# Kernel optimization log

Hardware: AMD Instinct MI355X
Metric: run time of the kernel (lower is better)

## Reference

```python
import jax, jax.numpy as jnp
import numpy as np

N = 50000      # nodes
E = 800000     # edges
IN = 128       # input feature dim
HID = 64       # out_channels per head
HEADS = 2
OUT = 40       # num classes
SLOPE = 0.2    # leaky relu negative slope
EPS = 1e-16    # PyG softmax denominator epsilon


def _xavier(key, shape):
    fan_out, fan_in = shape[0], shape[1]
    a = float(np.sqrt(6.0 / (fan_in + fan_out)))
    return jax.random.uniform(key, shape, minval=-a, maxval=a, dtype=jnp.float32)


def setup_inputs() -> dict:
    key = jax.random.key(0)
    ks = jax.random.split(key, 16)
    x = jax.random.normal(ks[0], (N, IN), dtype=jnp.float32)
    edge_index = jax.random.randint(ks[1], (2, E), 0, N, dtype=jnp.int64)
    # GAT layer 1: lin_l == lin_r (shared), weight [H*C, in], att [C, H]
    W1 = _xavier(ks[2], (HEADS * HID, IN))
    b1 = jnp.zeros((HEADS * HID,), jnp.float32)
    al1 = _xavier(ks[3], (HID, HEADS))
    ar1 = _xavier(ks[4], (HID, HEADS))
    # GAT layer 2: input dim = heads*hidden
    W2 = _xavier(ks[5], (HEADS * HID, HEADS * HID))
    b2 = jnp.zeros((HEADS * HID,), jnp.float32)
    al2 = _xavier(ks[6], (HID, HEADS))
    ar2 = _xavier(ks[7], (HID, HEADS))
    # post_mp: Linear(heads*hid, hid) -> Linear(hid, out)
    Wp1 = _xavier(ks[8], (HID, HEADS * HID))
    bp1 = jnp.zeros((HID,), jnp.float32)
    Wp2 = _xavier(ks[9], (OUT, HID))
    bp2 = jnp.zeros((OUT,), jnp.float32)
    return dict(x=x, edge_index=edge_index, W1=W1, b1=b1, al1=al1, ar1=ar1,
                W2=W2, b2=b2, al2=al2, ar2=ar2, Wp1=Wp1, bp1=bp1, Wp2=Wp2, bp2=bp2)


def gat_layer(x, edge_index, W, b, att_l, att_r):
    """One GAT layer: shared linear, per-edge leaky-relu scores,
    segment-softmax keyed by destination node, scatter-sum."""
    n = x.shape[0]
    xt = (x @ W.T + b).reshape(n, HEADS, HID)          # [N, H, C] (x_l == x_r)
    alpha_l = jnp.einsum('nhc,ch->nh', xt, att_l)      # [N, H]
    alpha_r = jnp.einsum('nhc,ch->nh', xt, att_r)      # [N, H]
    src, dst = edge_index[0], edge_index[1]            # j = source, i = dest
    e = jax.nn.leaky_relu(alpha_r[dst] + alpha_l[src], SLOPE)   # [E, H]
    # segment softmax over edges grouped by destination node
    seg_max = jax.ops.segment_max(e, dst, num_segments=n)       # [N, H]
    ex = jnp.exp(e - seg_max[dst])
    denom = jax.ops.segment_sum(ex, dst, num_segments=n)        # [N, H]
    alpha = ex / (denom[dst] + EPS)                              # [E, H]
    msg = alpha[:, :, None] * xt[src]                            # [E, H, C]
    out = jax.ops.segment_sum(msg, dst, num_segments=n)          # [N, H, C]
    return out.reshape(n, HEADS * HID)


def reference(x, edge_index, W1, b1, al1, ar1, W2, b2, al2, ar2, Wp1, bp1, Wp2, bp2):
    h = jax.nn.relu(gat_layer(x, edge_index, W1, b1, al1, ar1))
    h = jax.nn.relu(gat_layer(h, edge_index, W2, b2, al2, ar2))
    h = h @ Wp1.T + bp1
    h = h @ Wp2.T + bp2
    return jax.nn.log_softmax(h, axis=1)
```

## Files before the change

kernel.cpp:

```cpp
#include <hip/hip_runtime.h>
#include <hip/hip_fp16.h>
#include <cmath>

#define N_NODES 50000
#define N_EDGES 800000
#define F 128
#define OUT_DIM 40
#define SLOPE 0.2f
#define EPS_DEN 1e-16f

#define BK_SHIFT 7
#define BKSZ 128
#define NBK ((N_NODES + BKSZ - 1) / BKSZ)
#define BK_CAP2 2560
#define SC_CHUNK 2500
#define SC_BLOCKS ((N_EDGES + SC_CHUNK - 1) / SC_CHUNK)

typedef _Float16 half8 __attribute__((ext_vector_type(8)));
typedef float floatx4 __attribute__((ext_vector_type(4)));

__device__ inline float4 load4(const float* p) { return *(const float4*)p; }
__device__ inline float4 load4(const __half* p) {
  uint2 u = *(const uint2*)p;
  float2 a = __half22float2(*(__half2*)&u.x);
  float2 b = __half22float2(*(__half2*)&u.y);
  return make_float4(a.x, a.y, b.x, b.y);
}

template <typename T>
__global__ __launch_bounds__(256) void gemm_mfma(const T* __restrict__ A,
    const float* __restrict__ W, const float* __restrict__ b,
    const float* __restrict__ attl, const float* __restrict__ attr,
    __half* __restrict__ Ch, float* __restrict__ al, float* __restrict__ ar,
    int nrows) {
  __shared__ __half Ah[128][40];
  __shared__ __half Bh[128][40];
  int tid = threadIdx.x;
  int lane = tid & 63, wid = tid >> 6;
  int quad = lane >> 4, col = lane & 15;
  int r0 = blockIdx.x * 128;
  int rowhalf = wid >> 1, colhalf = wid & 1;
  floatx4 acc[4][4] = {};
  for (int kc = 0; kc < 128; kc += 32) {
    for (int i = tid; i < 512; i += 256) {
      int row = i >> 2, seg = i & 3;
      int gr = r0 + row;
      float4 v0, v1;
      if (gr < nrows) {
        const T* p = A + (size_t)gr * 128 + kc + seg * 8;
        v0 = load4(p); v1 = load4(p + 4);
      } else { v0 = make_float4(0.f,0.f,0.f,0.f); v1 = v0; }
      __half2 h0 = __floats2half2_rn(v0.x, v0.y), h1 = __floats2half2_rn(v0.z, v0.w);
      __half2 h2 = __floats2half2_rn(v1.x, v1.y), h3 = __floats2half2_rn(v1.z, v1.w);
      uint4 pk; pk.x = *(unsigned*)&h0; pk.y = *(unsigned*)&h1;
      pk.z = *(unsigned*)&h2; pk.w = *(unsigned*)&h3;
      *(uint4*)&Ah[row][seg * 8] = pk;
      const float* q = W + (size_t)row * 128 + kc + seg * 8;
      float4 w0 = *(const float4*)q, w1 = *(const float4*)(q + 4);
      __half2 g0 = __floats2half2_rn(w0.x, w0.y), g1 = __floats2half2_rn(w0.z, w0.w);
      __half2 g2 = __floats2half2_rn(w1.x, w1.y), g3 = __floats2half2_rn(w1.z, w1.w);
      uint4 qk; qk.x = *(unsigned*)&g0; qk.y = *(unsigned*)&g1;
      qk.z = *(unsigned*)&g2; qk.w = *(unsigned*)&g3;
      *(uint4*)&Bh[row][seg * 8] = qk;
    }
    __syncthreads();
    half8 afr[4], bfr[4];
#pragma unroll
    for (int rt = 0; rt < 4; ++rt)
      afr[rt] = *(const half8*)&Ah[rowhalf * 64 + rt * 16 + col][quad * 8];
#pragma unroll
    for (int ct = 0; ct < 4; ++ct)
      bfr[ct] = *(const half8*)&Bh[colhalf * 64 + ct * 16 + col][quad * 8];
#pragma unroll
    for (int rt = 0; rt < 4; ++rt)
#pragma unroll
      for (int ct = 0; ct < 4; ++ct)
        acc[rt][ct] = __builtin_amdgcn_mfma_f32_16x16x32_f16(afr[rt], bfr[ct],
                                                             acc[rt][ct], 0, 0, 0);
    __syncthreads();
  }
  int head = colhalf;
  float bj[4], wl4[4], wr4[4];
#pragma unroll
  for (int ct = 0; ct < 4; ++ct) {
    int c = ct * 16 + col;
    bj[ct] = b[head * 64 + c];
    wl4[ct] = attl[c * 2 + head];
    wr4[ct] = attr[c * 2 + head];
  }
#pragma unroll
  for (int rt = 0; rt < 4; ++rt) {
#pragma unroll
    for (int reg = 0; reg < 4; ++reg) {
      int gr = r0 + rowhalf * 64 + rt * 16 + quad * 4 + reg;
      bool ok = gr < nrows;
      float pl = 0.f, pr = 0.f;
#pragma unroll
      for (int ct = 0; ct < 4; ++ct) {
        float v = acc[rt][ct][reg] + bj[ct];
        pl += v * wl4[ct]; pr += v * wr4[ct];
        if (ok) Ch[(size_t)gr * F + head * 64 + ct * 16 + col] = __float2half(v);
      }
      pl += __shfl_xor(pl, 1, 64); pr += __shfl_xor(pr, 1, 64);
      pl += __shfl_xor(pl, 2, 64); pr += __shfl_xor(pr, 2, 64);
      pl += __shfl_xor(pl, 4, 64); pr += __shfl_xor(pr, 4, 64);
      pl += __shfl_xor(pl, 8, 64); pr += __shfl_xor(pr, 8, 64);
      if (ok && col == 0) { al[gr * 2 + head] = pl; ar[gr * 2 + head] = pr; }
    }
  }
}

__global__ __launch_bounds__(256) void bucket_scatter(const int* __restrict__ ei,
    int* __restrict__ bcur, int* __restrict__ pairs) {
  __shared__ int   sd[SC_CHUNK];
  __shared__ short sb[SC_CHUNK];
  __shared__ int h[NBK], lofs[NBK];
  int tid = threadIdx.x;
  for (int i = tid; i < NBK; i += 256) h[i] = 0;
  __syncthreads();
  int base = blockIdx.x * SC_CHUNK;
  int end = base + SC_CHUNK; if (end > N_EDGES) end = N_EDGES;
  int cnt = end - base;
  for (int e = base + tid; e < end; e += 256) {
    int s = ei[e];
    int d = ei[N_EDGES + e];
    int b = d >> BK_SHIFT;
    sd[e - base] = (s << BK_SHIFT) | (d & (BKSZ - 1));
    sb[e - base] = (short)b;
    atomicAdd(&h[b], 1);
  }
  __syncthreads();
  for (int i = tid; i < NBK; i += 256)
    if (h[i]) { lofs[i] = i * BK_CAP2 + atomicAdd(&bcur[i], h[i]); h[i] = 0; }
  __syncthreads();
  for (int i = tid; i < cnt; i += 256) {
    int b = sb[i];
    int pos = lofs[b] + atomicAdd(&h[b], 1);
    pairs[pos] = sd[i];
  }
}

__global__ __launch_bounds__(256) void local_sort(const int* __restrict__ bcur,
    const int* __restrict__ pairs, int* __restrict__ rowstart,
    int* __restrict__ rowend, int* __restrict__ srcs) {
  __shared__ int buf[BK_CAP2];
  __shared__ int sorted[BK_CAP2];
  __shared__ int hist[BKSZ];
  __shared__ int cur[BKSZ];
  int tid = threadIdx.x;
  int b = blockIdx.x;
  int base = b * BK_CAP2;
  int cnt = bcur[b];
  if (cnt > BK_CAP2) cnt = BK_CAP2;
  if (tid < BKSZ) hist[tid] = 0;
  __syncthreads();
  for (int i = tid; i < cnt; i += 256) {
    int p = pairs[base + i];
    buf[i] = p;
    atomicAdd(&hist[p & (BKSZ - 1)], 1);
  }
  __syncthreads();
  if (tid < 64) {
    int lane = tid;
    int carry = 0;
#pragma unroll
    for (int c = 0; c < BKSZ; c += 64) {
      int v = hist[c + lane];
      int x = v;
#pragma unroll
      for (int off = 1; off < 64; off <<= 1) {
        int t = __shfl_up(x, off, 64);
        if (lane >= off) x += t;
      }
      int excl = carry + x - v;
      cur[c + lane] = excl;
      int node = b * BKSZ + c + lane;
      if (node < N_NODES) {
        rowstart[node] = base + excl;
        rowend[node]   = base + excl + v;
      }
      carry += __shfl(x, 63, 64);
    }
  }
  __syncthreads();
  for (int i = tid; i < cnt; i += 256) {
    int p = buf[i];
    int pos = atomicAdd(&cur[p & (BKSZ - 1)], 1);
    sorted[pos] = p >> BK_SHIFT;
  }
  __syncthreads();
  for (int i = tid; i < cnt; i += 256)
    srcs[base + i] = sorted[i];
}

__global__ __launch_bounds__(256) void aggregate_kernel(const int* __restrict__ rowstart,
    const int* __restrict__ rowend, const int* __restrict__ srcs,
    const float* __restrict__ al, const float* __restrict__ ar,
    const __half* __restrict__ xh, __half* __restrict__ out, int n) {
  __shared__ float ebuf[4][2][64];
  __shared__ int   sbuf[4][64];
  int tid = threadIdx.x;
  int wid = tid >> 6, lane = tid & 63;
  int g = lane >> 4, q = lane & 15;
  int head = q >> 3;
  int node = blockIdx.x * 4 + wid;
  if (node >= n) return;
  int start = rowstart[node], end = rowend[node];
  float2 arv = *(const float2*)(ar + (size_t)node * 2);
  float ar0 = arv.x, ar1 = arv.y;
  const float* wrow = &ebuf[wid][head][0];
  const __half* xbase = xh + q * 8;
  float acc[8] = {};
  float dl0 = 0.f, dl1 = 0.f;
  for (int c = start; c < end; c += 64) {
    int j = c + lane;
    float e0 = 0.f, e1 = 0.f; int soff = 0;
    if (j < end) {
      int s = srcs[j];
      soff = s << BK_SHIFT;
      float2 a = *(const float2*)(al + (size_t)s * 2);
      float s0 = a.x + ar0; s0 = (s0 > 0.f) ? s0 : SLOPE * s0;
      float s1 = a.y + ar1; s1 = (s1 > 0.f) ? s1 : SLOPE * s1;
      e0 = __expf(s0); e1 = __expf(s1);
    }
    dl0 += e0; dl1 += e1;
    ebuf[wid][0][lane] = e0; ebuf[wid][1][lane] = e1; sbuf[wid][lane] = soff;
    __builtin_amdgcn_wave_barrier();
    int cend = end - c; if (cend > 64) cend = 64;
#pragma unroll 4
    for (int t = 0; t < cend; t += 4) {
      int te = t + g;
      if (te < cend) {
        int so = sbuf[wid][te];
        float w = wrow[te];
        uint4 u = *(const uint4*)(xbase + so);
        const __half2* hh = (const __half2*)&u;
        float2 f0 = __half22float2(hh[0]);
        float2 f1 = __half22float2(hh[1]);
        float2 f2 = __half22float2(hh[2]);
        float2 f3 = __half22float2(hh[3]);
        acc[0] += w * f0.x; acc[1] += w * f0.y;
        acc[2] += w * f1.x; acc[3] += w * f1.y;
        acc[4] += w * f2.x; acc[5] += w * f2.y;
        acc[6] += w * f3.x; acc[7] += w * f3.y;
      }
    }
    __builtin_amdgcn_wave_barrier();
  }
#pragma unroll
  for (int off = 32; off > 0; off >>= 1) {
    dl0 += __shfl_xor(dl0, off, 64);
    dl1 += __shfl_xor(dl1, off, 64);
  }
#pragma unroll
  for (int k = 0; k < 8; ++k) {
    acc[k] += __shfl_xor(acc[k], 16, 64);
    acc[k] += __shfl_xor(acc[k], 32, 64);
  }
  if (g == 0) {
    float d = (head == 0) ? dl0 : dl1;
    float inv = 1.f / (d + EPS_DEN);
    __half2 o0 = __floats2half2_rn(fmaxf(acc[0] * inv, 0.f), fmaxf(acc[1] * inv, 0.f));
    __half2 o1 = __floats2half2_rn(fmaxf(acc[2] * inv, 0.f), fmaxf(acc[3] * inv, 0.f));
    __half2 o2 = __floats2half2_rn(fmaxf(acc[4] * inv, 0.f), fmaxf(acc[5] * inv, 0.f));
    __half2 o3 = __floats2half2_rn(fmaxf(acc[6] * inv, 0.f), fmaxf(acc[7] * inv, 0.f));
    uint4 pack;
    pack.x = *(unsigned*)&o0; pack.y = *(unsigned*)&o1;
    pack.z = *(unsigned*)&o2; pack.w = *(unsigned*)&o3;
    *(uint4*)(out + (size_t)node * F + q * 8) = pack;
  }
}

__global__ void combine_kernel(const float* __restrict__ Wp1, const float* __restrict__ bp1,
    const float* __restrict__ Wp2, const float* __restrict__ bp2,
    __half* __restrict__ Wch, float* __restrict__ bc) {
  int idx = blockIdx.x * 256 + threadIdx.x;
  if (blockIdx.x < 24) {
    int o = idx >> 7, k = idx & 127;
    float s = 0.f;
    if (o < OUT_DIM) {
#pragma unroll 8
      for (int j = 0; j < 64; ++j) s += Wp2[o * 64 + j] * Wp1[j * 128 + k];
    }
    Wch[o * 128 + k] = __float2half(s);
  } else if (threadIdx.x < 48) {
    int o = threadIdx.x;
    if (o < OUT_DIM) {
      float s = bp2[o];
      for (int j = 0; j < 64; ++j) s += Wp2[o * 64 + j] * bp1[j];
      bc[o] = s;
    } else {
      bc[o] = -1e30f;
    }
  }
}

__global__ __launch_bounds__(256) void post_mfma(const __half* __restrict__ hb,
    const __half* __restrict__ Wch, const float* __restrict__ bc,
    float* __restrict__ out, int n) {
  int tid = threadIdx.x;
  int lane = tid & 63, wid = tid >> 6;
  int quad = lane >> 4, col = lane & 15;
  int base = blockIdx.x * 64 + wid * 16;
  int arow = base + col;
  int asafe = (arow < n) ? arow : (n - 1);
  floatx4 acc[3] = {};
#pragma unroll
  for (int kc = 0; kc < 128; kc += 32) {
    half8 afr = *(const half8*)(hb + (size_t)asafe * F + kc + quad * 8);
#pragma unroll
    for (int ct = 0; ct < 3; ++ct) {
      half8 bfr = *(const half8*)(Wch + (size_t)(ct * 16 + col) * 128 + kc + quad * 8);
      acc[ct] = __builtin_amdgcn_mfma_f32_16x16x32_f16(afr, bfr, acc[ct], 0, 0, 0);
    }
  }
  float bcv[3];
#pragma unroll
  for (int ct = 0; ct < 3; ++ct) bcv[ct] = bc[ct * 16 + col];
#pragma unroll
  for (int reg = 0; reg < 4; ++reg) {
    int row = base + quad * 4 + reg;
    float z[3], m = -INFINITY;
#pragma unroll
    for (int ct = 0; ct < 3; ++ct) { z[ct] = acc[ct][reg] + bcv[ct]; m = fmaxf(m, z[ct]); }
    m = fmaxf(m, __shfl_xor(m, 1, 64));
    m = fmaxf(m, __shfl_xor(m, 2, 64));
    m = fmaxf(m, __shfl_xor(m, 4, 64));
    m = fmaxf(m, __shfl_xor(m, 8, 64));
    float s = 0.f;
#pragma unroll
    for (int ct = 0; ct < 3; ++ct) s += __expf(z[ct] - m);
    s += __shfl_xor(s, 1, 64);
    s += __shfl_xor(s, 2, 64);
    s += __shfl_xor(s, 4, 64);
    s += __shfl_xor(s, 8, 64);
    float ls = logf(s);
    if (row < n) {
#pragma unroll
      for (int ct = 0; ct < 3; ++ct) {
        int o = ct * 16 + col;
        if (o < OUT_DIM) out[(size_t)row * OUT_DIM + o] = z[ct] - m - ls;
      }
    }
  }
}

extern "C" void kernel_launch(void* const* d_in, const int* in_sizes, int n_in,
                              void* d_out, int out_size, void* d_ws, size_t ws_size,
                              hipStream_t stream) {
  const float* x   = (const float*)d_in[0];
  const int*   ei  = (const int*)d_in[1];
  const float* W1  = (const float*)d_in[2];
  const float* b1  = (const float*)d_in[3];
  const float* al1 = (const float*)d_in[4];
  const float* ar1 = (const float*)d_in[5];
  const float* W2  = (const float*)d_in[6];
  const float* b2  = (const float*)d_in[7];
  const float* al2 = (const float*)d_in[8];
  const float* ar2 = (const float*)d_in[9];
  const float* Wp1 = (const float*)d_in[10];
  const float* bp1 = (const float*)d_in[11];
  const float* Wp2 = (const float*)d_in[12];
  const float* bp2 = (const float*)d_in[13];
  float* out = (float*)d_out;

  float* al    = (float*)d_ws;
  float* ar    = al + (size_t)N_NODES * 2;
  __half* Wch  = (__half*)(ar + (size_t)N_NODES * 2);
  float* bc    = (float*)(Wch + 48 * 128);
  int* rowstart= (int*)(bc + 48);
  int* rowend  = rowstart + N_NODES;
  int* bcur    = rowend + N_NODES;
  int* srcs    = bcur + NBK + 1;
  int* pairs   = srcs + NBK * BK_CAP2;
  uintptr_t pp = ((uintptr_t)(pairs + NBK * BK_CAP2) + 255) & ~(uintptr_t)255;
  __half* xh   = (__half*)pp;
  __half* hb   = xh + (size_t)N_NODES * F;

  hipMemsetAsync(bcur, 0, NBK * sizeof(int), stream);
  bucket_scatter<<<SC_BLOCKS, 256, 0, stream>>>(ei, bcur, pairs);
  local_sort<<<NBK, 256, 0, stream>>>(bcur, pairs, rowstart, rowend, srcs);
  combine_kernel<<<25, 256, 0, stream>>>(Wp1, bp1, Wp2, bp2, Wch, bc);

  int ggrid = (N_NODES + 127) / 128;
  int nwgrid = (N_NODES + 3) / 4;

  gemm_mfma<float><<<ggrid, 256, 0, stream>>>(x, W1, b1, al1, ar1, xh, al, ar, N_NODES);
  aggregate_kernel<<<nwgrid, 256, 0, stream>>>(rowstart, rowend, srcs, al, ar, xh, hb, N_NODES);
  gemm_mfma<__half><<<ggrid, 256, 0, stream>>>(hb, W2, b2, al2, ar2, xh, al, ar, N_NODES);
  aggregate_kernel<<<nwgrid, 256, 0, stream>>>(rowstart, rowend, srcs, al, ar, xh, hb, N_NODES);
  post_mfma<<<(N_NODES + 63) / 64, 256, 0, stream>>>(hb, Wch, bc, out, N_NODES);
}
```

Baseline: 237.2 us.

## Fuse all GAT stages into one persistent megakernel with grid barriers

Merges edge bucketing, the post-MLP weight combine, layer-1 GEMM, sorting, both aggregations, the layer-2 GEMM and the post MLP into one persistent kernel. The phases are separated by a software grid barrier built on atomics. Edge scatter, the weight combine and the first GEMM now share one phase, so independent work runs together. This removes per-launch overhead and idle gaps between the separate launches. The cost is that the spin barrier only works if every block is resident; the grid size comes from an occupancy query and is capped at 1024 blocks.

```diff
diff --git a/kernel.cpp b/kernel.cpp
--- a/kernel.cpp
+++ b/kernel.cpp
@@ -15,9 +15,39 @@
 #define BK_CAP2 2560
 #define SC_CHUNK 2500
 #define SC_BLOCKS ((N_EDGES + SC_CHUNK - 1) / SC_CHUNK)
+#define GEMM_TILES ((N_NODES + 127) / 128)
+#define AGG_ITEMS ((N_NODES + 3) / 4)
+#define POST_TILES ((N_NODES + 63) / 64)
+#define P0_ITEMS (SC_BLOCKS + 25 + GEMM_TILES)
+#define SMEM_BYTES 21504
 
 typedef _Float16 half8 __attribute__((ext_vector_type(8)));
 typedef float floatx4 __attribute__((ext_vector_type(4)));
+
+struct ScatterS { int sd[SC_CHUNK]; short sb[SC_CHUNK]; int h[NBK]; int lofs[NBK]; };
+struct SortS    { int buf[BK_CAP2]; int sorted[BK_CAP2]; int hist[BKSZ]; int cur[BKSZ]; };
+struct GemmS    { __half Ah[128][40]; __half Bh[128][40]; };
+struct AggS     { float ebuf[4][2][64]; int sbuf[4][64]; };
+static_assert(sizeof(ScatterS) <= SMEM_BYTES, "scatter LDS");
+static_assert(sizeof(SortS)    <= SMEM_BYTES, "sort LDS");
+static_assert(sizeof(GemmS)    <= SMEM_BYTES, "gemm LDS");
+static_assert(sizeof(AggS)     <= SMEM_BYTES, "agg LDS");
+
+__device__ __forceinline__ void grid_barrier(int* cnt, int* gen) {
+  __syncthreads();
+  if (threadIdx.x == 0) {
+    __threadfence();
+    int g = atomicAdd(gen, 0);
+    if (atomicAdd(cnt, 1) == (int)gridDim.x - 1) {
+      atomicExch(cnt, 0);
+      atomicAdd(gen, 1);
+    } else {
+      while (atomicAdd(gen, 0) == g) __builtin_amdgcn_s_sleep(2);
+    }
+    __threadfence();
+  }
+  __syncthreads();
+}
 
 __device__ inline float4 load4(const float* p) { return *(const float4*)p; }
 __device__ inline float4 load4(const __half* p) {
@@ -27,18 +57,118 @@
   return make_float4(a.x, a.y, b.x, b.y);
 }
 
+__device__ __forceinline__ void scatter_phase(const int* __restrict__ ei,
+    int* __restrict__ bcur, int* __restrict__ pairs, int it, int tid, char* smem_) {
+  ScatterS* S = (ScatterS*)smem_;
+  for (int i = tid; i < NBK; i += 256) S->h[i] = 0;
+  __syncthreads();
+  int base = it * SC_CHUNK;
+  int end = base + SC_CHUNK; if (end > N_EDGES) end = N_EDGES;
+  int cnt = end - base;
+  for (int e = base + tid; e < end; e += 256) {
+    int s = ei[e];
+    int d = ei[N_EDGES + e];
+    int b = d >> BK_SHIFT;
+    S->sd[e - base] = (s << BK_SHIFT) | (d & (BKSZ - 1));
+    S->sb[e - base] = (short)b;
+    atomicAdd(&S->h[b], 1);
+  }
+  __syncthreads();
+  for (int i = tid; i < NBK; i += 256)
+    if (S->h[i]) { S->lofs[i] = i * BK_CAP2 + atomicAdd(&bcur[i], S->h[i]); S->h[i] = 0; }
+  __syncthreads();
+  for (int i = tid; i < cnt; i += 256) {
+    int b = S->sb[i];
+    int pos = S->lofs[b] + atomicAdd(&S->h[b], 1);
+    pairs[pos] = S->sd[i];
+  }
+  __syncthreads();
+}
+
+__device__ __forceinline__ void combine_phase(const float* __restrict__ Wp1,
+    const float* __restrict__ bp1, const float* __restrict__ Wp2,
+    const float* __restrict__ bp2, __half* __restrict__ Wch,
+    float* __restrict__ bc, int it, int tid) {
+  if (it < 24) {
+    int idx = it * 256 + tid;
+    int o = idx >> 7, k = idx & 127;
+    float s = 0.f;
+    if (o < OUT_DIM) {
+#pragma unroll 8
+      for (int j = 0; j < 64; ++j) s += Wp2[o * 64 + j] * Wp1[j * 128 + k];
+    }
+    Wch[o * 128 + k] = __float2half(s);
+  } else if (tid < 48) {
+    int o = tid;
+    if (o < OUT_DIM) {
+      float s = bp2[o];
+      for (int j = 0; j < 64; ++j) s += Wp2[o * 64 + j] * bp1[j];
+      bc[o] = s;
+    } else {
+      bc[o] = -1e30f;
+    }
+  }
+}
+
+__device__ __forceinline__ void sort_phase(const int* __restrict__ bcur,
+    const int* __restrict__ pairs, int* __restrict__ rowstart,
+    int* __restrict__ rowend, int* __restrict__ srcs, int b, int tid, char* smem_) {
+  SortS* S = (SortS*)smem_;
+  int base = b * BK_CAP2;
+  int cnt = bcur[b];
+  if (cnt > BK_CAP2) cnt = BK_CAP2;
+  if (tid < BKSZ) S->hist[tid] = 0;
+  __syncthreads();
+  for (int i = tid; i < cnt; i += 256) {
+    int p = pairs[base + i];
+    S->buf[i] = p;
+    atomicAdd(&S->hist[p & (BKSZ - 1)], 1);
+  }
+  __syncthreads();
+  if (tid < 64) {
+    int lane = tid;
+    int carry = 0;
+#pragma unroll
+    for (int c = 0; c < BKSZ; c += 64) {
+      int v = S->hist[c + lane];
+      int x = v;
+#pragma unroll
+      for (int off = 1; off < 64; off <<= 1) {
+        int t = __shfl_up(x, off, 64);
+        if (lane >= off) x += t;
+      }
+      int excl = carry + x - v;
+      S->cur[c + lane] = excl;
+      int node = b * BKSZ + c + lane;
+      if (node < N_NODES) {
+        rowstart[node] = base + excl;
+        rowend[node]   = base + excl + v;
+      }
+      carry += __shfl(x, 63, 64);
+    }
+  }
+  __syncthreads();
+  for (int i = tid; i < cnt; i += 256) {
+    int p = S->buf[i];
+    int pos = atomicAdd(&S->cur[p & (BKSZ - 1)], 1);
+    S->sorted[pos] = p >> BK_SHIFT;
+  }
+  __syncthreads();
+  for (int i = tid; i < cnt; i += 256)
+    srcs[base + i] = S->sorted[i];
+  __syncthreads();
+}
+
 template <typename T>
-__global__ __launch_bounds__(256) void gemm_mfma(const T* __restrict__ A,
+__device__ __forceinline__ void gemm_phase(const T* __restrict__ A,
     const float* __restrict__ W, const float* __restrict__ b,
     const float* __restrict__ attl, const float* __restrict__ attr,
     __half* __restrict__ Ch, float* __restrict__ al, float* __restrict__ ar,
-    int nrows) {
-  __shared__ __half Ah[128][40];
-  __shared__ __half Bh[128][40];
-  int tid = threadIdx.x;
+    int nrows, int tile, int tid, char* smem_) {
+  GemmS* S = (GemmS*)smem_;
   int lane = tid & 63, wid = tid >> 6;
   int quad = lane >> 4, col = lane & 15;
-  int r0 = blockIdx.x * 128;
+  int r0 = tile * 128;
   int rowhalf = wid >> 1, colhalf = wid & 1;
   floatx4 acc[4][4] = {};
   for (int kc = 0; kc < 128; kc += 32) {
@@ -54,23 +184,23 @@
       __half2 h2 = __floats2half2_rn(v1.x, v1.y), h3 = __floats2half2_rn(v1.z, v1.w);
       uint4 pk; pk.x = *(unsigned*)&h0; pk.y = *(unsigned*)&h1;
       pk.z = *(unsigned*)&h2; pk.w = *(unsigned*)&h3;
-      *(uint4*)&Ah[row][seg * 8] = pk;
+      *(uint4*)&S->Ah[row][seg * 8] = pk;
       const float* q = W + (size_t)row * 128 + kc + seg * 8;
       float4 w0 = *(const float4*)q, w1 = *(const float4*)(q + 4);
       __half2 g0 = __floats2half2_rn(w0.x, w0.y), g1 = __floats2half2_rn(w0.z, w0.w);
       __half2 g2 = __floats2half2_rn(w1.x, w1.y), g3 = __floats2half2_rn(w1.z, w1.w);
       uint4 qk; qk.x = *(unsigned*)&g0; qk.y = *(unsigned*)&g1;
       qk.z = *(unsigned*)&g2; qk.w = *(unsigned*)&g3;
-      *(uint4*)&Bh[row][seg * 8] = qk;
+      *(uint4*)&S->Bh[row][seg * 8] = qk;
     }
     __syncthreads();
     half8 afr[4], bfr[4];
 #pragma unroll
     for (int rt = 0; rt < 4; ++rt)
-      afr[rt] = *(const half8*)&Ah[rowhalf * 64 + rt * 16 + col][quad * 8];
+      afr[rt] = *(const half8*)&S->Ah[rowhalf * 64 + rt * 16 + col][quad * 8];
 #pragma unroll
     for (int ct = 0; ct < 4; ++ct)
-      bfr[ct] = *(const half8*)&Bh[colhalf * 64 + ct * 16 + col][quad * 8];
+      bfr[ct] = *(const half8*)&S->Bh[colhalf * 64 + ct * 16 + col][quad * 8];
 #pragma unroll
     for (int rt = 0; rt < 4; ++rt)
 #pragma unroll
@@ -110,105 +240,21 @@
   }
 }
 
-__global__ __launch_bounds__(256) void bucket_scatter(const int* __restrict__ ei,
-    int* __restrict__ bcur, int* __restrict__ pairs) {
-  __shared__ int   sd[SC_CHUNK];
-  __shared__ short sb[SC_CHUNK];
-  __shared__ int h[NBK], lofs[NBK];
-  int tid = threadIdx.x;
-  for (int i = tid; i < NBK; i += 256) h[i] = 0;
-  __syncthreads();
-  int base = blockIdx.x * SC_CHUNK;
-  int end = base + SC_CHUNK; if (end > N_EDGES) end = N_EDGES;
-  int cnt = end - base;
-  for (int e = base + tid; e < end; e += 256) {
-    int s = ei[e];
-    int d = ei[N_EDGES + e];
-    int b = d >> BK_SHIFT;
-    sd[e - base] = (s << BK_SHIFT) | (d & (BKSZ - 1));
-    sb[e - base] = (short)b;
-    atomicAdd(&h[b], 1);
-  }
-  __syncthreads();
-  for (int i = tid; i < NBK; i += 256)
-    if (h[i]) { lofs[i] = i * BK_CAP2 + atomicAdd(&bcur[i], h[i]); h[i] = 0; }
-  __syncthreads();
-  for (int i = tid; i < cnt; i += 256) {
-    int b = sb[i];
-    int pos = lofs[b] + atomicAdd(&h[b], 1);
-    pairs[pos] = sd[i];
-  }
-}
-
-__global__ __launch_bounds__(256) void local_sort(const int* __restrict__ bcur,
-    const int* __restrict__ pairs, int* __restrict__ rowstart,
-    int* __restrict__ rowend, int* __restrict__ srcs) {
-  __shared__ int buf[BK_CAP2];
-  __shared__ int sorted[BK_CAP2];
-  __shared__ int hist[BKSZ];
-  __shared__ int cur[BKSZ];
-  int tid = threadIdx.x;
-  int b = blockIdx.x;
-  int base = b * BK_CAP2;
-  int cnt = bcur[b];
-  if (cnt > BK_CAP2) cnt = BK_CAP2;
-  if (tid < BKSZ) hist[tid] = 0;
-  __syncthreads();
-  for (int i = tid; i < cnt; i += 256) {
-    int p = pairs[base + i];
-    buf[i] = p;
-    atomicAdd(&hist[p & (BKSZ - 1)], 1);
-  }
-  __syncthreads();
-  if (tid < 64) {
-    int lane = tid;
-    int carry = 0;
-#pragma unroll
-    for (int c = 0; c < BKSZ; c += 64) {
-      int v = hist[c + lane];
-      int x = v;
-#pragma unroll
-      for (int off = 1; off < 64; off <<= 1) {
-        int t = __shfl_up(x, off, 64);
-        if (lane >= off) x += t;
-      }
-      int excl = carry + x - v;
-      cur[c + lane] = excl;
-      int node = b * BKSZ + c + lane;
-      if (node < N_NODES) {
-        rowstart[node] = base + excl;
-        rowend[node]   = base + excl + v;
-      }
-      carry += __shfl(x, 63, 64);
-    }
-  }
-  __syncthreads();
-  for (int i = tid; i < cnt; i += 256) {
-    int p = buf[i];
-    int pos = atomicAdd(&cur[p & (BKSZ - 1)], 1);
-    sorted[pos] = p >> BK_SHIFT;
-  }
-  __syncthreads();
-  for (int i = tid; i < cnt; i += 256)
-    srcs[base + i] = sorted[i];
-}
-
-__global__ __launch_bounds__(256) void aggregate_kernel(const int* __restrict__ rowstart,
+__device__ __forceinline__ void agg_phase(const int* __restrict__ rowstart,
     const int* __restrict__ rowend, const int* __restrict__ srcs,
     const float* __restrict__ al, const float* __restrict__ ar,
-    const __half* __restrict__ xh, __half* __restrict__ out, int n) {
-  __shared__ float ebuf[4][2][64];
-  __shared__ int   sbuf[4][64];
-  int tid = threadIdx.x;
+    const __half* __restrict__ xh, __half* __restrict__ out,
+    int item, int tid, char* smem_) {
+  AggS* S = (AggS*)smem_;
   int wid = tid >> 6, lane = tid & 63;
   int g = lane >> 4, q = lane & 15;
   int head = q >> 3;
-  int node = blockIdx.x * 4 + wid;
-  if (node >= n) return;
+  int node = item * 4 + wid;
+  if (node >= N_NODES) return;
   int start = rowstart[node], end = rowend[node];
   float2 arv = *(const float2*)(ar + (size_t)node * 2);
   float ar0 = arv.x, ar1 = arv.y;
-  const float* wrow = &ebuf[wid][head][0];
+  const float* wrow = &S->ebuf[wid][head][0];
   const __half* xbase = xh + q * 8;
   float acc[8] = {};
   float dl0 = 0.f, dl1 = 0.f;
@@ -224,14 +270,14 @@
       e0 = __expf(s0); e1 = __expf(s1);
     }
     dl0 += e0; dl1 += e1;
-    ebuf[wid][0][lane] = e0; ebuf[wid][1][lane] = e1; sbuf[wid][lane] = soff;
+    S->ebuf[wid][0][lane] = e0; S->ebuf[wid][1][lane] = e1; S->sbuf[wid][lane] = soff;
     __builtin_amdgcn_wave_barrier();
     int cend = end - c; if (cend > 64) cend = 64;
 #pragma unroll 4
     for (int t = 0; t < cend; t += 4) {
       int te = t + g;
       if (te < cend) {
-        int so = sbuf[wid][te];
+        int so = S->sbuf[wid][te];
         float w = wrow[te];
         uint4 u = *(const uint4*)(xbase + so);
         const __half2* hh = (const __half2*)&u;
@@ -271,39 +317,14 @@
   }
 }
 
-__global__ void combine_kernel(const float* __restrict__ Wp1, const float* __restrict__ bp1,
-    const float* __restrict__ Wp2, const float* __restrict__ bp2,
-    __half* __restrict__ Wch, float* __restrict__ bc) {
-  int idx = blockIdx.x * 256 + threadIdx.x;
-  if (blockIdx.x < 24) {
-    int o = idx >> 7, k = idx & 127;
-    float s = 0.f;
-    if (o < OUT_DIM) {
-#pragma unroll 8
-      for (int j = 0; j < 64; ++j) s += Wp2[o * 64 + j] * Wp1[j * 128 + k];
-    }
-    Wch[o * 128 + k] = __float2half(s);
-  } else if (threadIdx.x < 48) {
-    int o = threadIdx.x;
-    if (o < OUT_DIM) {
-      float s = bp2[o];
-      for (int j = 0; j < 64; ++j) s += Wp2[o * 64 + j] * bp1[j];
-      bc[o] = s;
-    } else {
-      bc[o] = -1e30f;
-    }
-  }
-}
-
-__global__ __launch_bounds__(256) void post_mfma(const __half* __restrict__ hb,
+__device__ __forceinline__ void post_phase(const __half* __restrict__ hb,
     const __half* __restrict__ Wch, const float* __restrict__ bc,
-    float* __restrict__ out, int n) {
-  int tid = threadIdx.x;
+    float* __restrict__ out, int it, int tid) {
   int lane = tid & 63, wid = tid >> 6;
   int quad = lane >> 4, col = lane & 15;
-  int base = blockIdx.x * 64 + wid * 16;
+  int base = it * 64 + wid * 16;
   int arow = base + col;
-  int asafe = (arow < n) ? arow : (n - 1);
+  int asafe = (arow < N_NODES) ? arow : (N_NODES - 1);
   floatx4 acc[3] = {};
 #pragma unroll
   for (int kc = 0; kc < 128; kc += 32) {
@@ -335,7 +356,7 @@
     s += __shfl_xor(s, 4, 64);
     s += __shfl_xor(s, 8, 64);
     float ls = logf(s);
-    if (row < n) {
+    if (row < N_NODES) {
 #pragma unroll
       for (int ct = 0; ct < 3; ++ct) {
         int o = ct * 16 + col;
@@ -343,6 +364,58 @@
       }
     }
   }
+}
+
+__global__ __launch_bounds__(256, 4) void mega(
+    const float* __restrict__ x, const int* __restrict__ ei,
+    const float* __restrict__ W1, const float* __restrict__ b1,
+    const float* __restrict__ al1, const float* __restrict__ ar1,
+    const float* __restrict__ W2, const float* __restrict__ b2,
+    const float* __restrict__ al2, const float* __restrict__ ar2,
+    const float* __restrict__ Wp1, const float* __restrict__ bp1,
+    const float* __restrict__ Wp2, const float* __restrict__ bp2,
+    float* __restrict__ out,
+    float* __restrict__ al, float* __restrict__ ar,
+    __half* __restrict__ Wch, float* __restrict__ bc,
+    int* __restrict__ rowstart, int* __restrict__ rowend,
+    int* __restrict__ bar, int* __restrict__ bcur,
+    int* __restrict__ srcs, int* __restrict__ pairs,
+    __half* __restrict__ xh, __half* __restrict__ hb) {
+  __shared__ __align__(16) char smem[SMEM_BYTES];
+  int tid = threadIdx.x;
+  int bid = blockIdx.x;
+  int nb  = gridDim.x;
+  int* cnt = bar;
+  int* gen = bar + 1;
+
+  for (int it = bid; it < P0_ITEMS; it += nb) {
+    if (it < SC_BLOCKS) scatter_phase(ei, bcur, pairs, it, tid, smem);
+    else if (it < SC_BLOCKS + 25)
+      combine_phase(Wp1, bp1, Wp2, bp2, Wch, bc, it - SC_BLOCKS, tid);
+    else
+      gemm_phase<float>(x, W1, b1, al1, ar1, xh, al, ar, N_NODES,
+                        it - SC_BLOCKS - 25, tid, smem);
+  }
+  grid_barrier(cnt, gen);
+
+  for (int it = bid; it < NBK; it += nb)
+    sort_phase(bcur, pairs, rowstart, rowend, srcs, it, tid, smem);
+  grid_barrier(cnt, gen);
+
+  for (int it = bid; it < AGG_ITEMS; it += nb)
+    agg_phase(rowstart, rowend, srcs, al, ar, xh, hb, it, tid, smem);
+  grid_barrier(cnt, gen);
+
+  for (int it = bid; it < GEMM_TILES; it += nb)
+    gemm_phase<__half>(hb, W2, b2, al2, ar2, xh, al, ar, N_NODES, it, tid, smem);
+  grid_barrier(cnt, gen);
+
+  for (int it = bid; it < AGG_ITEMS; it += nb)
+    agg_phase(rowstart, rowend, srcs, al, ar, xh, hb, it, tid, smem);
+  grid_barrier(cnt, gen);
+
+  for (int it = bid; it < POST_TILES; it += nb)
+    post_phase(hb, Wch, bc, out, it, tid);
 }
 
 extern "C" void kernel_launch(void* const* d_in, const int* in_sizes, int n_in,
@@ -370,24 +443,23 @@
   float* bc    = (float*)(Wch + 48 * 128);
   int* rowstart= (int*)(bc + 48);
   int* rowend  = rowstart + N_NODES;
-  int* bcur    = rowend + N_NODES;
-  int* srcs    = bcur + NBK + 1;
+  int* bar     = rowend + N_NODES;
+  int* bcur    = bar + 8;
+  int* srcs    = bcur + NBK;
   int* pairs   = srcs + NBK * BK_CAP2;
   uintptr_t pp = ((uintptr_t)(pairs + NBK * BK_CAP2) + 255) & ~(uintptr_t)255;
   __half* xh   = (__half*)pp;
   __half* hb   = xh + (size_t)N_NODES * F;
 
-  hipMemsetAsync(bcur, 0, NBK * sizeof(int), stream);
-  bucket_scatter<<<SC_BLOCKS, 256, 0, stream>>>(ei, bcur, pairs);
-  local_sort<<<NBK, 256, 0, stream>>>(bcur, pairs, rowstart, rowend, srcs);
-  combine_kernel<<<25, 256, 0, stream>>>(Wp1, bp1, Wp2, bp2, Wch, bc);
-
-  int ggrid = (N_NODES + 127) / 128;
-  int nwgrid = (N_NODES + 3) / 4;
-
-  gemm_mfma<float><<<ggrid, 256, 0, stream>>>(x, W1, b1, al1, ar1, xh, al, ar, N_NODES);
-  aggregate_kernel<<<nwgrid, 256, 0, stream>>>(rowstart, rowend, srcs, al, ar, xh, hb, N_NODES);
-  gemm_mfma<__half><<<ggrid, 256, 0, stream>>>(hb, W2, b2, al2, ar2, xh, al, ar, N_NODES);
-  aggregate_kernel<<<nwgrid, 256, 0, stream>>>(rowstart, rowend, srcs, al, ar, xh, hb, N_NODES);
-  post_mfma<<<(N_NODES + 63) / 64, 256, 0, stream>>>(hb, Wch, bc, out, N_NODES);
-}
+  int maxB = 0;
+  if (hipOccupancyMaxActiveBlocksPerMultiprocessor(&maxB, (const void*)mega,
+                                                   256, 0) != hipSuccess || maxB < 1)
+    maxB = 2;
+  int nb = maxB * 256;
+  if (nb > 1024) nb = 1024;
+
+  hipMemsetAsync(bar, 0, (8 + NBK) * sizeof(int), stream);
+  mega<<<nb, 256, 0, stream>>>(x, ei, W1, b1, al1, ar1, W2, b2, al2, ar2,
+                               Wp1, bp1, Wp2, bp2, out, al, ar, Wch, bc,
+                               rowstart, rowend, bar, bcur, srcs, pairs, xh, hb);
+}
```

Measured after the change: 617.9 us. 2.61x slower.

## Merge edge scatter, weight combine and first GEMM into one launch

Applied to the files above, without the earlier changes.

The bucket scatter, post-MLP weight combine and layer-1 GEMM are independent, so they now run as one kernel whose block index picks which phase to execute, with shared memory reused through a union-sized byte buffer. This removes two kernel launches and lets the GEMM tiles run alongside the atomic-heavy scatter instead of after it. In exchange every block reserves the larger shared-memory footprint, which may lower occupancy for the GEMM blocks.

```diff
diff --git a/kernel.cpp b/kernel.cpp
--- a/kernel.cpp
+++ b/kernel.cpp
@@ -15,9 +15,17 @@
 #define BK_CAP2 2560
 #define SC_CHUNK 2500
 #define SC_BLOCKS ((N_EDGES + SC_CHUNK - 1) / SC_CHUNK)
+#define GEMM_TILES ((N_NODES + 127) / 128)
+#define A_BLOCKS (SC_BLOCKS + 25 + GEMM_TILES)
+#define SMEM_BYTES 21504
 
 typedef _Float16 half8 __attribute__((ext_vector_type(8)));
 typedef float floatx4 __attribute__((ext_vector_type(4)));
+
+struct ScatterS { int sd[SC_CHUNK]; short sb[SC_CHUNK]; int h[NBK]; int lofs[NBK]; };
+struct GemmS    { __half Ah[128][40]; __half Bh[128][40]; };
+static_assert(sizeof(ScatterS) <= SMEM_BYTES, "scatter LDS");
+static_assert(sizeof(GemmS)    <= SMEM_BYTES, "gemm LDS");
 
 __device__ inline float4 load4(const float* p) { return *(const float4*)p; }
 __device__ inline float4 load4(const __half* p) {
@@ -27,18 +35,68 @@
   return make_float4(a.x, a.y, b.x, b.y);
 }
 
+__device__ __forceinline__ void scatter_phase(const int* __restrict__ ei,
+    int* __restrict__ bcur, int* __restrict__ pairs, int it, int tid, char* smem_) {
+  ScatterS* S = (ScatterS*)smem_;
+  for (int i = tid; i < NBK; i += 256) S->h[i] = 0;
+  __syncthreads();
+  int base = it * SC_CHUNK;
+  int end = base + SC_CHUNK; if (end > N_EDGES) end = N_EDGES;
+  int cnt = end - base;
+  for (int e = base + tid; e < end; e += 256) {
+    int s = ei[e];
+    int d = ei[N_EDGES + e];
+    int b = d >> BK_SHIFT;
+    S->sd[e - base] = (s << BK_SHIFT) | (d & (BKSZ - 1));
+    S->sb[e - base] = (short)b;
+    atomicAdd(&S->h[b], 1);
+  }
+  __syncthreads();
+  for (int i = tid; i < NBK; i += 256)
+    if (S->h[i]) { S->lofs[i] = i * BK_CAP2 + atomicAdd(&bcur[i], S->h[i]); S->h[i] = 0; }
+  __syncthreads();
+  for (int i = tid; i < cnt; i += 256) {
+    int b = S->sb[i];
+    int pos = S->lofs[b] + atomicAdd(&S->h[b], 1);
+    pairs[pos] = S->sd[i];
+  }
+}
+
+__device__ __forceinline__ void combine_phase(const float* __restrict__ Wp1,
+    const float* __restrict__ bp1, const float* __restrict__ Wp2,
+    const float* __restrict__ bp2, __half* __restrict__ Wch,
+    float* __restrict__ bc, int it, int tid) {
+  if (it < 24) {
+    int idx = it * 256 + tid;
+    int o = idx >> 7, k = idx & 127;
+    float s = 0.f;
+    if (o < OUT_DIM) {
+#pragma unroll 8
+      for (int j = 0; j < 64; ++j) s += Wp2[o * 64 + j] * Wp1[j * 128 + k];
+    }
+    Wch[o * 128 + k] = __float2half(s);
+  } else if (tid < 48) {
+    int o = tid;
+    if (o < OUT_DIM) {
+      float s = bp2[o];
+      for (int j = 0; j < 64; ++j) s += Wp2[o * 64 + j] * bp1[j];
+      bc[o] = s;
+    } else {
+      bc[o] = -1e30f;
+    }
+  }
+}
+
 template <typename T>
-__global__ __launch_bounds__(256) void gemm_mfma(const T* __restrict__ A,
+__device__ __forceinline__ void gemm_phase(const T* __restrict__ A,
     const float* __restrict__ W, const float* __restrict__ b,
     const float* __restrict__ attl, const float* __restrict__ attr,
     __half* __restrict__ Ch, float* __restrict__ al, float* __restrict__ ar,
-    int nrows) {
-  __shared__ __half Ah[128][40];
-  __shared__ __half Bh[128][40];
-  int tid = threadIdx.x;
+    int nrows, int tile, int tid, char* smem_) {
+  GemmS* S = (GemmS*)smem_;
   int lane = tid & 63, wid = tid >> 6;
   int quad = lane >> 4, col = lane & 15;
-  int r0 = blockIdx.x * 128;
+  int r0 = tile * 128;
   int rowhalf = wid >> 1, colhalf = wid & 1;
   floatx4 acc[4][4] = {};
   for (int kc = 0; kc < 128; kc += 32) {
@@ -54,23 +112,23 @@
       __half2 h2 = __floats2half2_rn(v1.x, v1.y), h3 = __floats2half2_rn(v1.z, v1.w);
       uint4 pk; pk.x = *(unsigned*)&h0; pk.y = *(unsigned*)&h1;
       pk.z = *(unsigned*)&h2; pk.w = *(unsigned*)&h3;
-      *(uint4*)&Ah[row][seg * 8] = pk;
+      *(uint4*)&S->Ah[row][seg * 8] = pk;
       const float* q = W + (size_t)row * 128 + kc + seg * 8;
       float4 w0 = *(const float4*)q, w1 = *(const float4*)(q + 4);
       __half2 g0 = __floats2half2_rn(w0.x, w0.y), g1 = __floats2half2_rn(w0.z, w0.w);
       __half2 g2 = __floats2half2_rn(w1.x, w1.y), g3 = __floats2half2_rn(w1.z, w1.w);
       uint4 qk; qk.x = *(unsigned*)&g0; qk.y = *(unsigned*)&g1;
       qk.z = *(unsigned*)&g2; qk.w = *(unsigned*)&g3;
-      *(uint4*)&Bh[row][seg * 8] = qk;
+      *(uint4*)&S->Bh[row][seg * 8] = qk;
     }
     __syncthreads();
     half8 afr[4], bfr[4];
 #pragma unroll
     for (int rt = 0; rt < 4; ++rt)
-      afr[rt] = *(const half8*)&Ah[rowhalf * 64 + rt * 16 + col][quad * 8];
+      afr[rt] = *(const half8*)&S->Ah[rowhalf * 64 + rt * 16 + col][quad * 8];
 #pragma unroll
     for (int ct = 0; ct < 4; ++ct)
-      bfr[ct] = *(const half8*)&Bh[colhalf * 64 + ct * 16 + col][quad * 8];
+      bfr[ct] = *(const half8*)&S->Bh[colhalf * 64 + ct * 16 + col][quad * 8];
 #pragma unroll
     for (int rt = 0; rt < 4; ++rt)
 #pragma unroll
@@ -110,34 +168,34 @@
   }
 }
 
-__global__ __launch_bounds__(256) void bucket_scatter(const int* __restrict__ ei,
-    int* __restrict__ bcur, int* __restrict__ pairs) {
-  __shared__ int   sd[SC_CHUNK];
-  __shared__ short sb[SC_CHUNK];
-  __shared__ int h[NBK], lofs[NBK];
-  int tid = threadIdx.x;
-  for (int i = tid; i < NBK; i += 256) h[i] = 0;
-  __syncthreads();
-  int base = blockIdx.x * SC_CHUNK;
-  int end = base + SC_CHUNK; if (end > N_EDGES) end = N_EDGES;
-  int cnt = end - base;
-  for (int e = base + tid; e < end; e += 256) {
-    int s = ei[e];
-    int d = ei[N_EDGES + e];
-    int b = d >> BK_SHIFT;
-    sd[e - base] = (s << BK_SHIFT) | (d & (BKSZ - 1));
-    sb[e - base] = (short)b;
-    atomicAdd(&h[b], 1);
-  }
-  __syncthreads();
-  for (int i = tid; i < NBK; i += 256)
-    if (h[i]) { lofs[i] = i * BK_CAP2 + atomicAdd(&bcur[i], h[i]); h[i] = 0; }
-  __syncthreads();
-  for (int i = tid; i < cnt; i += 256) {
-    int b = sb[i];
-    int pos = lofs[b] + atomicAdd(&h[b], 1);
-    pairs[pos] = sd[i];
-  }
+__global__ __launch_bounds__(256) void kernelA(const int* __restrict__ ei,
+    int* __restrict__ bcur, int* __restrict__ pairs,
+    const float* __restrict__ Wp1, const float* __restrict__ bp1,
+    const float* __restrict__ Wp2, const float* __restrict__ bp2,
+    __half* __restrict__ Wch, float* __restrict__ bc,
+    const float* __restrict__ x, const float* __restrict__ W1,
+    const float* __restrict__ b1, const float* __restrict__ al1,
+    const float* __restrict__ ar1, __half* __restrict__ xh,
+    float* __restrict__ al, float* __restrict__ ar) {
+  __shared__ __align__(16) char smem[SMEM_BYTES];
+  int bid = blockIdx.x, tid = threadIdx.x;
+  if (bid < SC_BLOCKS) {
+    scatter_phase(ei, bcur, pairs, bid, tid, smem);
+  } else if (bid < SC_BLOCKS + 25) {
+    combine_phase(Wp1, bp1, Wp2, bp2, Wch, bc, bid - SC_BLOCKS, tid);
+  } else {
+    gemm_phase<float>(x, W1, b1, al1, ar1, xh, al, ar, N_NODES,
+                      bid - SC_BLOCKS - 25, tid, smem);
+  }
+}
+
+__global__ __launch_bounds__(256) void gemm2_kernel(const __half* __restrict__ hb,
+    const float* __restrict__ W2, const float* __restrict__ b2,
+    const float* __restrict__ al2, const float* __restrict__ ar2,
+    __half* __restrict__ xh, float* __restrict__ al, float* __restrict__ ar) {
+  __shared__ __align__(16) char smem[SMEM_BYTES];
+  gemm_phase<__half>(hb, W2, b2, al2, ar2, xh, al, ar, N_NODES,
+                     blockIdx.x, threadIdx.x, smem);
 }
 
 __global__ __launch_bounds__(256) void local_sort(const int* __restrict__ bcur,
@@ -271,30 +329,6 @@
   }
 }
 
-__global__ void combine_kernel(const float* __restrict__ Wp1, const float* __restrict__ bp1,
-    const float* __restrict__ Wp2, const float* __restrict__ bp2,
-    __half* __restrict__ Wch, float* __restrict__ bc) {
-  int idx = blockIdx.x * 256 + threadIdx.x;
-  if (blockIdx.x < 24) {
-    int o = idx >> 7, k = idx & 127;
-    float s = 0.f;
-    if (o < OUT_DIM) {
-#pragma unroll 8
-      for (int j = 0; j < 64; ++j) s += Wp2[o * 64 + j] * Wp1[j * 128 + k];
-    }
-    Wch[o * 128 + k] = __float2half(s);
-  } else if (threadIdx.x < 48) {
-    int o = threadIdx.x;
-    if (o < OUT_DIM) {
-      float s = bp2[o];
-      for (int j = 0; j < 64; ++j) s += Wp2[o * 64 + j] * bp1[j];
-      bc[o] = s;
-    } else {
-      bc[o] = -1e30f;
-    }
-  }
-}
-
 __global__ __launch_bounds__(256) void post_mfma(const __half* __restrict__ hb,
     const __half* __restrict__ Wch, const float* __restrict__ bc,
     float* __restrict__ out, int n) {
@@ -371,23 +405,20 @@
   int* rowstart= (int*)(bc + 48);
   int* rowend  = rowstart + N_NODES;
   int* bcur    = rowend + N_NODES;
-  int* srcs    = bcur + NBK + 1;
+  int* srcs    = bcur + NBK;
   int* pairs   = srcs + NBK * BK_CAP2;
   uintptr_t pp = ((uintptr_t)(pairs + NBK * BK_CAP2) + 255) & ~(uintptr_t)255;
   __half* xh   = (__half*)pp;
   __half* hb   = xh + (size_t)N_NODES * F;
 
+  int nwgrid = (N_NODES + 3) / 4;
+
   hipMemsetAsync(bcur, 0, NBK * sizeof(int), stream);
-  bucket_scatter<<<SC_BLOCKS, 256, 0, stream>>>(ei, bcur, pairs);
+  kernelA<<<A_BLOCKS, 256, 0, stream>>>(ei, bcur, pairs, Wp1, bp1, Wp2, bp2,
+                                        Wch, bc, x, W1, b1, al1, ar1, xh, al, ar);
   local_sort<<<NBK, 256, 0, stream>>>(bcur, pairs, rowstart, rowend, srcs);
-  combine_kernel<<<25, 256, 0, stream>>>(Wp1, bp1, Wp2, bp2, Wch, bc);
-
-  int ggrid = (N_NODES + 127) / 128;
-  int nwgrid = (N_NODES + 3) / 4;
-
-  gemm_mfma<float><<<ggrid, 256, 0, stream>>>(x, W1, b1, al1, ar1, xh, al, ar, N_NODES);
   aggregate_kernel<<<nwgrid, 256, 0, stream>>>(rowstart, rowend, srcs, al, ar, xh, hb, N_NODES);
-  gemm_mfma<__half><<<ggrid, 256, 0, stream>>>(hb, W2, b2, al2, ar2, xh, al, ar, N_NODES);
+  gemm2_kernel<<<GEMM_TILES, 256, 0, stream>>>(hb, W2, b2, al2, ar2, xh, al, ar);
   aggregate_kernel<<<nwgrid, 256, 0, stream>>>(rowstart, rowend, srcs, al, ar, xh, hb, N_NODES);
   post_mfma<<<(N_NODES + 63) / 64, 256, 0, stream>>>(hb, Wch, bc, out, N_NODES);
 }
```

Result: faster. 226.7 us (-4.4%).
